# Optimization experiments

Measured on AMD Instinct MI355X. Metric: run time of the kernel, lower is better.

## Reference

```python
import jax, jax.numpy as jnp
from jax import lax
import numpy as np

B, T, DD, DS, H = 512, 365, 5, 27, 256


def setup_inputs() -> dict:
    key = jax.random.key(0)
    ks = jax.random.split(key, 12)
    s = lambda fan_in: 1.0 / np.sqrt(fan_in)
    return {
        "x_dynamic": jax.random.normal(ks[0], (B, T, DD), jnp.float32),
        "x_static": jax.random.normal(ks[1], (B, DS), jnp.float32),
        "Wi": jax.random.normal(ks[2], (DS, H), jnp.float32) * s(DS),
        "bi": jax.random.normal(ks[3], (H,), jnp.float32) * s(DS),
        "Wf": jax.random.normal(ks[4], (DS, H), jnp.float32) * s(DS),
        "bf": jax.random.normal(ks[5], (H,), jnp.float32) * s(DS),
        "Wg": jax.random.normal(ks[6], (DD + H, H), jnp.float32) * s(DD + H),
        "bg": jax.random.normal(ks[7], (H,), jnp.float32) * s(DD + H),
        "Wo": jax.random.normal(ks[8], (DD + H, H), jnp.float32) * s(DD + H),
        "bo": jax.random.normal(ks[9], (H,), jnp.float32) * s(DD + H),
        "Wh": jax.random.normal(ks[10], (H, 1), jnp.float32) * s(H),
        "bh": jax.random.normal(ks[11], (1,), jnp.float32) * s(H),
    }


def reference(x_dynamic, x_static, Wi, bi, Wf, bf, Wg, bg, Wo, bo, Wh, bh):
    # Entity-aware gates depend only on static input -> compute once, reuse every step.
    i = jax.nn.sigmoid(x_static @ Wi + bi)  # [B, H]
    f = jax.nn.sigmoid(x_static @ Wf + bf)  # [B, H]

    bsz = x_dynamic.shape[0]
    hid = Wi.shape[1]
    h0 = jnp.zeros((bsz, hid), x_dynamic.dtype)
    c0 = jnp.zeros((bsz, hid), x_dynamic.dtype)

    def step(carry, x_t):
        h, c = carry
        comb = jnp.concatenate([x_t, h], axis=1)          # [B, DD+H]
        g = jnp.tanh(comb @ Wg + bg)
        o = jax.nn.sigmoid(comb @ Wo + bo)
        c_next = f * c + i * g
        h_next = o * jnp.tanh(c_next)
        return (h_next, c_next), None

    xs = jnp.swapaxes(x_dynamic, 0, 1)  # [T, B, DD]
    (h, _), _ = lax.scan(step, (h0, c0), xs)

    # Dropout is identity in eval mode.
    return h @ Wh + bh  # [B, 1]
```

## Files before the change

### kernel.cpp

```cpp
#include <hip/hip_runtime.h>

#define B_   512
#define T_   365
#define DD_  5
#define DS_  27
#define H_   256
#define ROWS 2
#define NBLK (B_ / ROWS)
#define NW   8
#define NTHR (NW * 64)

typedef _Float16 half8_t __attribute__((ext_vector_type(8)));
typedef float    f32x4   __attribute__((ext_vector_type(4)));

#define LOG2E_ 1.4426950408889634f

__device__ __forceinline__ float sigmoid_f(float x) {
    return __builtin_amdgcn_rcpf(1.0f + __builtin_amdgcn_exp2f(-x * LOG2E_));
}
__device__ __forceinline__ float tanh_f(float x) {
    return 1.0f - 2.0f * __builtin_amdgcn_rcpf(1.0f + __builtin_amdgcn_exp2f(2.0f * LOG2E_ * x));
}

__global__ __launch_bounds__(NTHR, 2)
void ealstm_kernel(const float* __restrict__ xdyn,
                   const float* __restrict__ xstat,
                   const float* __restrict__ Wi, const float* __restrict__ bi,
                   const float* __restrict__ Wf, const float* __restrict__ bf_,
                   const float* __restrict__ Wg, const float* __restrict__ bg,
                   const float* __restrict__ Wo, const float* __restrict__ bo,
                   const float* __restrict__ Wh, const float* __restrict__ bh,
                   float* __restrict__ out)
{
    const int tid = threadIdx.x;
    const int l   = tid & 63;
    const int w   = tid >> 6;
    const int b0  = blockIdx.x * ROWS;

    __shared__ __align__(16) _Float16 hbuf[2][16][264];
    __shared__ float xsh[ROWS][T_ * DD_];
    __shared__ float red[NW];

    {
        _Float16* hz = &hbuf[0][0][0];
        for (int i = tid; i < 2 * 16 * 264; i += NTHR) hz[i] = (_Float16)0.0f;
    }
    for (int i = tid; i < ROWS * T_ * DD_; i += NTHR) {
        int r   = i / (T_ * DD_);
        int rem = i - r * (T_ * DD_);
        xsh[r][rem] = xdyn[(size_t)(b0 + r) * (T_ * DD_) + rem];
    }

    const int colW = w * 32;
    const int lg   = l >> 4;
    const int lm   = l & 15;
    half8_t Bf[2][2][8];
    {
#pragma unroll
        for (int m = 0; m < 2; ++m) {
            const float* Ws = (m == 0) ? Wg : Wo;
#pragma unroll
            for (int tt = 0; tt < 2; ++tt) {
#pragma unroll
                for (int ks = 0; ks < 8; ++ks) {
                    int col = colW + tt * 16 + lm;
                    int k   = ks * 32 + 8 * lg;
                    const float* p = Ws + (size_t)(DD_ + k) * H_ + col;
                    half8_t v;
#pragma unroll
                    for (int i = 0; i < 8; ++i) v[i] = (_Float16)p[(size_t)i * H_];
                    Bf[m][tt][ks] = v;
                }
            }
        }
    }

    const int r_l = (l >> 4) & 1;
    const int ch  = l >> 5;
    const int c_l = colW + ch * 16 + lm;
    const int s_l = lm;

    float Wgx[DD_], Wox[DD_];
#pragma unroll
    for (int d = 0; d < DD_; ++d) {
        Wgx[d] = Wg[d * H_ + c_l];
        Wox[d] = Wo[d * H_ + c_l];
    }
    const float bgv = bg[c_l], bov = bo[c_l];

    float iG, fG, cst = 0.0f;
    {
        float ai = bi[c_l], af = bf_[c_l];
        for (int d = 0; d < DS_; ++d) {
            float xv = xstat[(b0 + r_l) * DS_ + d];
            ai += xv * Wi[d * H_ + c_l];
            af += xv * Wf[d * H_ + c_l];
        }
        iG = sigmoid_f(ai);
        fG = sigmoid_f(af);
    }

    half8_t Af[8];
    {
        half8_t z;
#pragma unroll
        for (int i = 0; i < 8; ++i) z[i] = (_Float16)0.0f;
#pragma unroll
        for (int ks = 0; ks < 8; ++ks) Af[ks] = z;
    }
    const bool areal = (lm < ROWS);

    __syncthreads();

    for (int t = 0; t < T_; ++t) {
        const int cur = t & 1;
        const int nxt = cur ^ 1;

        if (areal) {
#pragma unroll
            for (int ks = 0; ks < 8; ++ks)
                Af[ks] = *(const half8_t*)&hbuf[cur][lm][ks * 32 + 8 * lg];
        }

        float xg = bgv, xo = bov;
#pragma unroll
        for (int d = 0; d < DD_; ++d) {
            float xv = xsh[r_l][t * DD_ + d];
            xg += xv * Wgx[d];
            xo += xv * Wox[d];
        }

        f32x4 accG0 = {0.f,0.f,0.f,0.f}, accG1 = {0.f,0.f,0.f,0.f};
        f32x4 accO0 = {0.f,0.f,0.f,0.f}, accO1 = {0.f,0.f,0.f,0.f};
#pragma unroll
        for (int ks = 0; ks < 8; ++ks) {
            accG0 = __builtin_amdgcn_mfma_f32_16x16x32_f16(Af[ks], Bf[0][0][ks], accG0, 0, 0, 0);
            accG1 = __builtin_amdgcn_mfma_f32_16x16x32_f16(Af[ks], Bf[0][1][ks], accG1, 0, 0, 0);
            accO0 = __builtin_amdgcn_mfma_f32_16x16x32_f16(Af[ks], Bf[1][0][ks], accO0, 0, 0, 0);
            accO1 = __builtin_amdgcn_mfma_f32_16x16x32_f16(Af[ks], Bf[1][1][ks], accO1, 0, 0, 0);
        }

        float g00 = __shfl(accG0[0], s_l), g01 = __shfl(accG0[1], s_l);
        float g10 = __shfl(accG1[0], s_l), g11 = __shfl(accG1[1], s_l);
        float o00 = __shfl(accO0[0], s_l), o01 = __shfl(accO0[1], s_l);
        float o10 = __shfl(accO1[0], s_l), o11 = __shfl(accO1[1], s_l);
        float pg = ch ? (r_l ? g11 : g10) : (r_l ? g01 : g00);
        float po = ch ? (r_l ? o11 : o10) : (r_l ? o01 : o00);
        pg += xg;
        po += xo;

        float g = tanh_f(pg);
        float o = sigmoid_f(po);
        cst = fG * cst + iG * g;
        float hv = o * tanh_f(cst);
        hbuf[nxt][r_l][c_l] = (_Float16)hv;

        __syncthreads();
    }

    const int fin  = T_ & 1;
    const int oc   = tid & 255;
    const int orow = tid >> 8;
    float v = (float)hbuf[fin][orow][oc] * Wh[oc];
#pragma unroll
    for (int off = 32; off > 0; off >>= 1)
        v += __shfl_down(v, off);
    if (l == 0) red[w] = v;
    __syncthreads();
    if (tid < ROWS) {
        out[b0 + tid] = red[tid * 4 + 0] + red[tid * 4 + 1]
                      + red[tid * 4 + 2] + red[tid * 4 + 3] + bh[0];
    }
}

extern "C" void kernel_launch(void* const* d_in, const int* in_sizes, int n_in,
                              void* d_out, int out_size, void* d_ws, size_t ws_size,
                              hipStream_t stream) {
    (void)in_sizes; (void)n_in; (void)out_size; (void)d_ws; (void)ws_size;
    const float* xdyn  = (const float*)d_in[0];
    const float* xstat = (const float*)d_in[1];
    const float* Wi    = (const float*)d_in[2];
    const float* bi    = (const float*)d_in[3];
    const float* Wf    = (const float*)d_in[4];
    const float* bf    = (const float*)d_in[5];
    const float* Wg    = (const float*)d_in[6];
    const float* bg    = (const float*)d_in[7];
    const float* Wo    = (const float*)d_in[8];
    const float* bo    = (const float*)d_in[9];
    const float* Wh    = (const float*)d_in[10];
    const float* bh    = (const float*)d_in[11];
    float* out = (float*)d_out;

    hipLaunchKernelGGL(ealstm_kernel, dim3(NBLK), dim3(NTHR), 0, stream,
                       xdyn, xstat, Wi, bi, Wf, bf, Wg, bg, Wo, bo, Wh, bh, out);
}
```

Baseline: 310.2 us.

## Halve warps per block, give each warp 64 columns, overlap MFMA with gate math

Each block now runs 4 warps instead of 8, so each warp computes 64 hidden columns with twice as many MFMA tiles and register-resident weight fragments. The second set of MFMAs is split in two halves so the activation and cell update for the first column set run between them, hiding transcendental latency behind matrix work. The dynamic input is padded to 8 floats per step for a vectorised LDS read. Fewer warps per block means a cheaper per-step barrier, at the cost of doubled register pressure for the weight fragments and occupancy limited to one block per launch bound.

Result: slower. 390.3 us (+25.8%).

```diff
diff --git a/kernel.cpp b/kernel.cpp
--- a/kernel.cpp
+++ b/kernel.cpp
@@ -7,7 +7,7 @@
 #define H_   256
 #define ROWS 2
 #define NBLK (B_ / ROWS)
-#define NW   8
+#define NW   4
 #define NTHR (NW * 64)
 
 typedef _Float16 half8_t __attribute__((ext_vector_type(8)));
@@ -22,7 +22,7 @@
     return 1.0f - 2.0f * __builtin_amdgcn_rcpf(1.0f + __builtin_amdgcn_exp2f(2.0f * LOG2E_ * x));
 }
 
-__global__ __launch_bounds__(NTHR, 2)
+__global__ __launch_bounds__(NTHR, 1)
 void ealstm_kernel(const float* __restrict__ xdyn,
                    const float* __restrict__ xstat,
                    const float* __restrict__ Wi, const float* __restrict__ bi,
@@ -38,8 +38,8 @@
     const int b0  = blockIdx.x * ROWS;
 
     __shared__ __align__(16) _Float16 hbuf[2][16][264];
-    __shared__ float xsh[ROWS][T_ * DD_];
-    __shared__ float red[NW];
+    __shared__ __align__(16) float xsh[ROWS][T_][8];
+    __shared__ float red[2][NW];
 
     {
         _Float16* hz = &hbuf[0][0][0];
@@ -48,19 +48,21 @@
     for (int i = tid; i < ROWS * T_ * DD_; i += NTHR) {
         int r   = i / (T_ * DD_);
         int rem = i - r * (T_ * DD_);
-        xsh[r][rem] = xdyn[(size_t)(b0 + r) * (T_ * DD_) + rem];
-    }
-
-    const int colW = w * 32;
+        int tt  = rem / DD_;
+        int d   = rem - tt * DD_;
+        xsh[r][tt][d] = xdyn[(size_t)(b0 + r) * (T_ * DD_) + rem];
+    }
+
+    const int colW = w * 64;
     const int lg   = l >> 4;
     const int lm   = l & 15;
-    half8_t Bf[2][2][8];
+    half8_t Bf[2][4][8];
     {
 #pragma unroll
         for (int m = 0; m < 2; ++m) {
             const float* Ws = (m == 0) ? Wg : Wo;
 #pragma unroll
-            for (int tt = 0; tt < 2; ++tt) {
+            for (int tt = 0; tt < 4; ++tt) {
 #pragma unroll
                 for (int ks = 0; ks < 8; ++ks) {
                     int col = colW + tt * 16 + lm;
@@ -75,29 +77,34 @@
         }
     }
 
-    const int r_l = (l >> 4) & 1;
-    const int ch  = l >> 5;
-    const int c_l = colW + ch * 16 + lm;
-    const int s_l = lm;
-
-    float Wgx[DD_], Wox[DD_];
+    const int r_l  = (l >> 4) & 1;
+    const int tsel = l >> 5;
+    const int cA   = colW + tsel * 16 + lm;
+    const int cB   = cA + 32;
+
+    float WgxA[DD_], WoxA[DD_], WgxB[DD_], WoxB[DD_];
 #pragma unroll
     for (int d = 0; d < DD_; ++d) {
-        Wgx[d] = Wg[d * H_ + c_l];
-        Wox[d] = Wo[d * H_ + c_l];
-    }
-    const float bgv = bg[c_l], bov = bo[c_l];
-
-    float iG, fG, cst = 0.0f;
-    {
-        float ai = bi[c_l], af = bf_[c_l];
+        WgxA[d] = Wg[d * H_ + cA];
+        WoxA[d] = Wo[d * H_ + cA];
+        WgxB[d] = Wg[d * H_ + cB];
+        WoxB[d] = Wo[d * H_ + cB];
+    }
+    const float bgA = bg[cA], boA = bo[cA];
+    const float bgB = bg[cB], boB = bo[cB];
+
+    float iGA, fGA, cstA = 0.0f, iGB, fGB, cstB = 0.0f;
+    {
+        float aiA = bi[cA], afA = bf_[cA], aiB = bi[cB], afB = bf_[cB];
         for (int d = 0; d < DS_; ++d) {
             float xv = xstat[(b0 + r_l) * DS_ + d];
-            ai += xv * Wi[d * H_ + c_l];
-            af += xv * Wf[d * H_ + c_l];
-        }
-        iG = sigmoid_f(ai);
-        fG = sigmoid_f(af);
+            aiA += xv * Wi[d * H_ + cA];
+            afA += xv * Wf[d * H_ + cA];
+            aiB += xv * Wi[d * H_ + cB];
+            afB += xv * Wf[d * H_ + cB];
+        }
+        iGA = sigmoid_f(aiA);  fGA = sigmoid_f(afA);
+        iGB = sigmoid_f(aiB);  fGB = sigmoid_f(afB);
     }
 
     half8_t Af[8];
@@ -122,54 +129,85 @@
                 Af[ks] = *(const half8_t*)&hbuf[cur][lm][ks * 32 + 8 * lg];
         }
 
-        float xg = bgv, xo = bov;
-#pragma unroll
-        for (int d = 0; d < DD_; ++d) {
-            float xv = xsh[r_l][t * DD_ + d];
-            xg += xv * Wgx[d];
-            xo += xv * Wox[d];
-        }
-
-        f32x4 accG0 = {0.f,0.f,0.f,0.f}, accG1 = {0.f,0.f,0.f,0.f};
-        f32x4 accO0 = {0.f,0.f,0.f,0.f}, accO1 = {0.f,0.f,0.f,0.f};
+        const float4 xv = *(const float4*)&xsh[r_l][t][0];
+        const float  x4 = xsh[r_l][t][4];
+        float xgA = bgA + xv.x*WgxA[0] + xv.y*WgxA[1] + xv.z*WgxA[2] + xv.w*WgxA[3] + x4*WgxA[4];
+        float xoA = boA + xv.x*WoxA[0] + xv.y*WoxA[1] + xv.z*WoxA[2] + xv.w*WoxA[3] + x4*WoxA[4];
+        float xgB = bgB + xv.x*WgxB[0] + xv.y*WgxB[1] + xv.z*WgxB[2] + xv.w*WgxB[3] + x4*WgxB[4];
+        float xoB = boB + xv.x*WoxB[0] + xv.y*WoxB[1] + xv.z*WoxB[2] + xv.w*WoxB[3] + x4*WoxB[4];
+
+        f32x4 aG0 = {0.f,0.f,0.f,0.f}, aG1 = {0.f,0.f,0.f,0.f};
+        f32x4 aG2 = {0.f,0.f,0.f,0.f}, aG3 = {0.f,0.f,0.f,0.f};
+        f32x4 aO0 = {0.f,0.f,0.f,0.f}, aO1 = {0.f,0.f,0.f,0.f};
+        f32x4 aO2 = {0.f,0.f,0.f,0.f}, aO3 = {0.f,0.f,0.f,0.f};
+
 #pragma unroll
         for (int ks = 0; ks < 8; ++ks) {
-            accG0 = __builtin_amdgcn_mfma_f32_16x16x32_f16(Af[ks], Bf[0][0][ks], accG0, 0, 0, 0);
-            accG1 = __builtin_amdgcn_mfma_f32_16x16x32_f16(Af[ks], Bf[0][1][ks], accG1, 0, 0, 0);
-            accO0 = __builtin_amdgcn_mfma_f32_16x16x32_f16(Af[ks], Bf[1][0][ks], accO0, 0, 0, 0);
-            accO1 = __builtin_amdgcn_mfma_f32_16x16x32_f16(Af[ks], Bf[1][1][ks], accO1, 0, 0, 0);
-        }
-
-        float g00 = __shfl(accG0[0], s_l), g01 = __shfl(accG0[1], s_l);
-        float g10 = __shfl(accG1[0], s_l), g11 = __shfl(accG1[1], s_l);
-        float o00 = __shfl(accO0[0], s_l), o01 = __shfl(accO0[1], s_l);
-        float o10 = __shfl(accO1[0], s_l), o11 = __shfl(accO1[1], s_l);
-        float pg = ch ? (r_l ? g11 : g10) : (r_l ? g01 : g00);
-        float po = ch ? (r_l ? o11 : o10) : (r_l ? o01 : o00);
-        pg += xg;
-        po += xo;
-
-        float g = tanh_f(pg);
-        float o = sigmoid_f(po);
-        cst = fG * cst + iG * g;
-        float hv = o * tanh_f(cst);
-        hbuf[nxt][r_l][c_l] = (_Float16)hv;
-
+            aG0 = __builtin_amdgcn_mfma_f32_16x16x32_f16(Af[ks], Bf[0][0][ks], aG0, 0, 0, 0);
+            aO0 = __builtin_amdgcn_mfma_f32_16x16x32_f16(Af[ks], Bf[1][0][ks], aO0, 0, 0, 0);
+            aG1 = __builtin_amdgcn_mfma_f32_16x16x32_f16(Af[ks], Bf[0][1][ks], aG1, 0, 0, 0);
+            aO1 = __builtin_amdgcn_mfma_f32_16x16x32_f16(Af[ks], Bf[1][1][ks], aO1, 0, 0, 0);
+        }
+
+        float sg0a = __shfl(aG0[0], lm), sg1a = __shfl(aG0[1], lm);
+        float sg0b = __shfl(aG1[0], lm), sg1b = __shfl(aG1[1], lm);
+        float so0a = __shfl(aO0[0], lm), so1a = __shfl(aO0[1], lm);
+        float so0b = __shfl(aO1[0], lm), so1b = __shfl(aO1[1], lm);
+
+#pragma unroll
+        for (int ks = 0; ks < 4; ++ks) {
+            aG2 = __builtin_amdgcn_mfma_f32_16x16x32_f16(Af[ks], Bf[0][2][ks], aG2, 0, 0, 0);
+            aO2 = __builtin_amdgcn_mfma_f32_16x16x32_f16(Af[ks], Bf[1][2][ks], aO2, 0, 0, 0);
+            aG3 = __builtin_amdgcn_mfma_f32_16x16x32_f16(Af[ks], Bf[0][3][ks], aG3, 0, 0, 0);
+            aO3 = __builtin_amdgcn_mfma_f32_16x16x32_f16(Af[ks], Bf[1][3][ks], aO3, 0, 0, 0);
+        }
+
+        {
+            float pgA = (tsel ? (r_l ? sg1b : sg0b) : (r_l ? sg1a : sg0a)) + xgA;
+            float poA = (tsel ? (r_l ? so1b : so0b) : (r_l ? so1a : so0a)) + xoA;
+            float gA  = tanh_f(pgA);
+            float oA  = sigmoid_f(poA);
+            cstA = fGA * cstA + iGA * gA;
+            float hA = oA * tanh_f(cstA);
+            hbuf[nxt][r_l][cA] = (_Float16)hA;
+        }
+
+#pragma unroll
+        for (int ks = 4; ks < 8; ++ks) {
+            aG2 = __builtin_amdgcn_mfma_f32_16x16x32_f16(Af[ks], Bf[0][2][ks], aG2, 0, 0, 0);
+            aO2 = __builtin_amdgcn_mfma_f32_16x16x32_f16(Af[ks], Bf[1][2][ks], aO2, 0, 0, 0);
+            aG3 = __builtin_amdgcn_mfma_f32_16x16x32_f16(Af[ks], Bf[0][3][ks], aG3, 0, 0, 0);
+            aO3 = __builtin_amdgcn_mfma_f32_16x16x32_f16(Af[ks], Bf[1][3][ks], aO3, 0, 0, 0);
+        }
+
+        {
+            float tg0a = __shfl(aG2[0], lm), tg1a = __shfl(aG2[1], lm);
+            float tg0b = __shfl(aG3[0], lm), tg1b = __shfl(aG3[1], lm);
+            float to0a = __shfl(aO2[0], lm), to1a = __shfl(aO2[1], lm);
+            float to0b = __shfl(aO3[0], lm), to1b = __shfl(aO3[1], lm);
+            float pgB = (tsel ? (r_l ? tg1b : tg0b) : (r_l ? tg1a : tg0a)) + xgB;
+            float poB = (tsel ? (r_l ? to1b : to0b) : (r_l ? to1a : to0a)) + xoB;
+            float gB  = tanh_f(pgB);
+            float oB  = sigmoid_f(poB);
+            cstB = fGB * cstB + iGB * gB;
+            float hB = oB * tanh_f(cstB);
+            hbuf[nxt][r_l][cB] = (_Float16)hB;
+        }
         __syncthreads();
     }
 
-    const int fin  = T_ & 1;
-    const int oc   = tid & 255;
-    const int orow = tid >> 8;
-    float v = (float)hbuf[fin][orow][oc] * Wh[oc];
-#pragma unroll
-    for (int off = 32; off > 0; off >>= 1)
-        v += __shfl_down(v, off);
-    if (l == 0) red[w] = v;
+    const int fin = T_ & 1;
+    float v0 = (float)hbuf[fin][0][tid] * Wh[tid];
+    float v1 = (float)hbuf[fin][1][tid] * Wh[tid];
+#pragma unroll
+    for (int off = 32; off > 0; off >>= 1) {
+        v0 += __shfl_down(v0, off);
+        v1 += __shfl_down(v1, off);
+    }
+    if (l == 0) { red[0][w] = v0; red[1][w] = v1; }
     __syncthreads();
     if (tid < ROWS) {
-        out[b0 + tid] = red[tid * 4 + 0] + red[tid * 4 + 1]
-                      + red[tid * 4 + 2] + red[tid * 4 + 3] + bh[0];
+        out[b0 + tid] = red[tid][0] + red[tid][1] + red[tid][2] + red[tid][3] + bh[0];
     }
 }
 
```
